# Performance work log

Hardware: AMD Instinct MI355X
Metric: run time of the kernel (lower is better)

Reference implementation:

```python
import jax, jax.numpy as jnp
import numpy as np

B, N, DIM = 2, 2048, 512
HEADS, DIM_HEAD = 8, 64
INNER = HEADS * DIM_HEAD
SCALE = DIM_HEAD ** -0.5
ALPHA = 32.0 ** 2  # stable_softmax alpha


def setup_inputs() -> dict:
    key = jax.random.key(0)
    k1, k2, k3, k4 = jax.random.split(key, 4)
    x = jax.random.normal(k1, (B, N, DIM), dtype=jnp.float32)
    mask = jnp.ones((B, N), dtype=bool)
    # nn.Linear(dim, inner*3, bias=False) -> stored transposed for x @ W
    w_qkv = jax.random.normal(k2, (DIM, INNER * 3), dtype=jnp.float32) * (DIM ** -0.5)
    w_out = jax.random.normal(k3, (INNER, DIM), dtype=jnp.float32) * (INNER ** -0.5)
    b_out = jax.random.normal(k4, (DIM,), dtype=jnp.float32) * 0.01
    return {"x": x, "mask": mask, "w_qkv": w_qkv, "w_out": w_out, "b_out": b_out}


def stable_softmax(t, alpha=ALPHA):
    t = t / alpha
    t = t - jnp.max(t, axis=-1, keepdims=True)
    return jax.nn.softmax(t * alpha, axis=-1)


def reference(x, mask, w_qkv, w_out, b_out):
    b, n, _ = x.shape
    qkv = x @ w_qkv  # [b, n, 3*inner]
    q, k, v = jnp.split(qkv, 3, axis=-1)
    # 'b n (h d) -> b h n d'
    split_heads = lambda t: t.reshape(b, n, HEADS, DIM_HEAD).transpose(0, 2, 1, 3)
    q, k, v = split_heads(q), split_heads(k), split_heads(v)
    q = q * SCALE
    dots = jnp.einsum('bhid,bhjd->bhij', q, k)  # [b, h, n, n]
    mask_value = -jnp.finfo(dots.dtype).max
    # key padding mask: 'b j -> b 1 1 j'
    dots = jnp.where(mask[:, None, None, :], dots, mask_value)
    # causal mask: triu with offset j - i + 1 == 1 here
    causal = jnp.triu(jnp.ones((n, n), dtype=bool), k=1)
    dots = jnp.where(causal, mask_value, dots)
    attn = stable_softmax(dots)
    out = jnp.einsum('bhij,bhjd->bhid', attn, v)
    out = out.transpose(0, 2, 1, 3).reshape(b, n, INNER)  # 'b h n d -> b n (h d)'
    return out @ w_out + b_out
```

## Files before the change

kernel.cpp:

```cpp
#include <hip/hip_runtime.h>
#include <hip/hip_bf16.h>
#include <stdint.h>

#define B_ 2
#define N_ 2048
#define DIM_ 512
#define HEADS_ 8
#define DHEAD_ 64
#define INNER_ 512

typedef float f32x4 __attribute__((ext_vector_type(4)));
typedef float f32x16 __attribute__((ext_vector_type(16)));
typedef __bf16 bf16x8 __attribute__((ext_vector_type(8)));
typedef unsigned short us8 __attribute__((ext_vector_type(8)));
typedef unsigned int u32x4 __attribute__((ext_vector_type(4)));

static __device__ __forceinline__ unsigned short f2bf(float f) {
    union { float f; unsigned int u; } v; v.f = f;
    unsigned int r = v.u + 0x7fffu + ((v.u >> 16) & 1u);
    return (unsigned short)(r >> 16);
}

static __device__ __forceinline__ float exp2_fast(float x) {
    return __builtin_amdgcn_exp2f(x);
}

static __device__ __forceinline__ unsigned cvtpk(float lo, float hi) {
    unsigned r;
    asm("v_cvt_pk_bf16_f32 %0, %1, %2" : "=v"(r) : "v"(lo), "v"(hi));
    return r;
}

static __device__ __forceinline__ f32x4 mfma16(bf16x8 a, bf16x8 b, f32x4 c) {
    return __builtin_amdgcn_mfma_f32_16x16x32_bf16(a, b, c, 0, 0, 0);
}
static __device__ __forceinline__ f32x16 mfma32(bf16x8 a, bf16x8 b, f32x16 c) {
    return __builtin_amdgcn_mfma_f32_32x32x16_bf16(a, b, c, 0, 0, 0);
}

static __device__ __forceinline__ size_t qk_off(int bh, int n, int d) {
    int T = n >> 5, r = n & 31, c = d >> 4, s = d & 15;
    return ((((size_t)bh * 64 + T) * 4 + c) << 9) + (size_t)(((s >> 3) * 32 + r) * 8 + (s & 7));
}
static __device__ __forceinline__ size_t vt_off(int bh, int d, int n) {
    int tt = n >> 5, kv = n & 31;
    int mi = (kv >> 4) & 1, g = (kv >> 2) & 1;
    int jj = (kv & 3) + 4 * ((kv >> 3) & 1);
    int dblk = d >> 5;
    int lane = (d & 31) + 32 * g;
    return ((((size_t)bh * 64 + tt) * 2 + dblk) * 2 + mi) * 512 + (size_t)(lane * 8 + jj);
}

__global__ __launch_bounds__(256) void k_transpose_w(const float* __restrict__ wqkv,
                                                     const float* __restrict__ wout,
                                                     unsigned short* __restrict__ oqkv,
                                                     unsigned short* __restrict__ oout,
                                                     float qscale) {
    __shared__ float tile[32][33];
    const int tx = threadIdx.x & 31, ty = threadIdx.x >> 5;
    const bool isQ = blockIdx.y < 48;
    const float* in = isQ ? wqkv : wout;
    unsigned short* out = isQ ? oqkv : oout;
    const int N = isQ ? 1536 : 512;
    const int scale_cols = isQ ? 512 : 0;
    const int K = 512;
    const int k0 = blockIdx.x * 32, n0 = (isQ ? blockIdx.y : blockIdx.y - 48) * 32;
#pragma unroll
    for (int j = 0; j < 4; j++)
        tile[ty + 8 * j][tx] = in[(size_t)(k0 + ty + 8 * j) * N + n0 + tx];
    __syncthreads();
#pragma unroll
    for (int j = 0; j < 4; j++) {
        int n = n0 + ty + 8 * j;
        float v = tile[tx][ty + 8 * j];
        if (n < scale_cols) v *= qscale;
        out[(size_t)n * K + k0 + tx] = f2bf(v);
    }
}

template <int MODE>
__global__ __launch_bounds__(256) void k_gemm(const void* __restrict__ Av,
                                              const unsigned short* __restrict__ Bt,
                                              int K, int Ncols,
                                              float* __restrict__ Cf,
                                              const float* __restrict__ bias,
                                              unsigned short* __restrict__ Qb,
                                              unsigned short* __restrict__ Kb,
                                              unsigned short* __restrict__ Vt) {
    __shared__ unsigned short As[128 * 72];
    __shared__ unsigned short Bs[128 * 72];
    const int t = threadIdx.x;
    const int lane = t & 63;
    const int w = t >> 6;
    const int wy = w >> 1, wx = w & 1;
    const int lo = lane & 15, hi = lane >> 4;

    const int ncolb = Ncols >> 7;
    const int bid = blockIdx.x;
    const int wg = (bid & 7) * ((int)gridDim.x >> 3) + (bid >> 3);
    const int row0 = (wg / ncolb) * 128, col0 = (wg % ncolb) * 128;

    f32x4 acc[4][4];
#pragma unroll
    for (int m = 0; m < 4; m++)
#pragma unroll
        for (int n = 0; n < 4; n++) acc[m][n] = 0.f;

    for (int k0 = 0; k0 < K; k0 += 64) {
#pragma unroll
        for (int i = 0; i < 4; i++) {
            int chunk = t + i * 256;
            int r = chunk >> 3;
            int c = (chunk & 7) << 3;
            if (MODE == 0) {
                const float* Af = (const float*)Av;
                float4 v0 = *(const float4*)&Af[(size_t)(row0 + r) * K + k0 + c];
                float4 v1 = *(const float4*)&Af[(size_t)(row0 + r) * K + k0 + c + 4];
                us8 o;
                o[0] = f2bf(v0.x); o[1] = f2bf(v0.y); o[2] = f2bf(v0.z); o[3] = f2bf(v0.w);
                o[4] = f2bf(v1.x); o[5] = f2bf(v1.y); o[6] = f2bf(v1.z); o[7] = f2bf(v1.w);
                *(us8*)&As[r * 72 + c] = o;
            } else {
                const unsigned short* Ab = (const unsigned short*)Av;
                *(us8*)&As[r * 72 + c] = *(const us8*)&Ab[(size_t)(row0 + r) * K + k0 + c];
            }
            *(us8*)&Bs[r * 72 + c] = *(const us8*)&Bt[(size_t)(col0 + r) * K + k0 + c];
        }
        __syncthreads();
#pragma unroll
        for (int ks = 0; ks < 2; ks++) {
            bf16x8 af[4], bfr[4];
#pragma unroll
            for (int m = 0; m < 4; m++)
                af[m] = *(const bf16x8*)&As[(wy * 64 + m * 16 + lo) * 72 + ks * 32 + hi * 8];
#pragma unroll
            for (int n = 0; n < 4; n++)
                bfr[n] = *(const bf16x8*)&Bs[(wx * 64 + n * 16 + lo) * 72 + ks * 32 + hi * 8];
#pragma unroll
            for (int m = 0; m < 4; m++)
#pragma unroll
                for (int n = 0; n < 4; n++)
                    acc[m][n] = mfma16(af[m], bfr[n], acc[m][n]);
        }
        __syncthreads();
    }

#pragma unroll
    for (int m = 0; m < 4; m++) {
#pragma unroll
        for (int n = 0; n < 4; n++) {
#pragma unroll
            for (int r = 0; r < 4; r++) {
                int row = row0 + wy * 64 + m * 16 + hi * 4 + r;
                int col = col0 + wx * 64 + n * 16 + lo;
                float v = acc[m][n][r];
                if (MODE == 0) {
                    unsigned short bv = f2bf(v);
                    int b = row >> 11, nn = row & 2047;
                    int sec = col >> 9, cc = col & 511;
                    int h = cc >> 6, d = cc & 63;
                    int bh = b * HEADS_ + h;
                    if (sec == 0)      Qb[qk_off(bh, nn, d)] = bv;
                    else if (sec == 1) Kb[qk_off(bh, nn, d)] = bv;
                    else               Vt[vt_off(bh, d, nn)] = bv;
                } else {
                    Cf[(size_t)row * Ncols + col] = v + bias[col];
                }
            }
        }
    }
}


static __device__ __forceinline__ void pack_P(const f32x16& sT, bf16x8& P0, bf16x8& P1) {
    u32x4 pw0, pw1;
    pw0[0] = cvtpk(sT[0], sT[1]);   pw0[1] = cvtpk(sT[2], sT[3]);
    pw0[2] = cvtpk(sT[4], sT[5]);   pw0[3] = cvtpk(sT[6], sT[7]);
    pw1[0] = cvtpk(sT[8], sT[9]);   pw1[1] = cvtpk(sT[10], sT[11]);
    pw1[2] = cvtpk(sT[12], sT[13]); pw1[3] = cvtpk(sT[14], sT[15]);
    P0 = __builtin_bit_cast(bf16x8, pw0);
    P1 = __builtin_bit_cast(bf16x8, pw1);
}

static __device__ __forceinline__ void do_tile(
    const unsigned short* kbase, const unsigned short* vbase, int tt,
    bool diag, int qg, int half,
    const bf16x8 (&qf)[4],
    float& m_, float& l_, f32x16& o0, f32x16& o1) {
    const unsigned short* kp = kbase + (size_t)tt * 2048;
    bf16x8 kf0 = *(const bf16x8*)(kp);
    bf16x8 kf1 = *(const bf16x8*)(kp + 512);
    bf16x8 kf2 = *(const bf16x8*)(kp + 1024);
    bf16x8 kf3 = *(const bf16x8*)(kp + 1536);
    const unsigned short* vp = vbase + (size_t)tt * 2048;
    bf16x8 vf00 = *(const bf16x8*)(vp);
    bf16x8 vf01 = *(const bf16x8*)(vp + 512);
    bf16x8 vf10 = *(const bf16x8*)(vp + 1024);
    bf16x8 vf11 = *(const bf16x8*)(vp + 1536);

    f32x16 sT = 0.f;
    sT = mfma32(kf0, qf[0], sT);
    sT = mfma32(kf1, qf[1], sT);
    sT = mfma32(kf2, qf[2], sT);
    sT = mfma32(kf3, qf[3], sT);

    if (diag) {
        const int kv0 = tt * 32;
#pragma unroll
        for (int r = 0; r < 16; r++) {
            int kv = kv0 + (r & 3) + 8 * (r >> 2) + 4 * half;
            if (kv > qg) sT[r] = -1e30f;
        }
    }

    float a0 = fmaxf(sT[0], sT[1]),  a1 = fmaxf(sT[2], sT[3]);
    float a2 = fmaxf(sT[4], sT[5]),  a3 = fmaxf(sT[6], sT[7]);
    float a4 = fmaxf(sT[8], sT[9]),  a5 = fmaxf(sT[10], sT[11]);
    float a6 = fmaxf(sT[12], sT[13]), a7 = fmaxf(sT[14], sT[15]);
    float mx = fmaxf(fmaxf(fmaxf(a0, a1), fmaxf(a2, a3)),
                     fmaxf(fmaxf(a4, a5), fmaxf(a6, a7)));

    bool need = __any(mx > m_ + 11.f);
    if (need) {
        mx = fmaxf(mx, __shfl_xor(mx, 32, 64));
        float mn = fmaxf(m_, mx);
        float al = exp2_fast(m_ - mn);
        m_ = mn;
        l_ *= al;
#pragma unroll
        for (int r = 0; r < 16; r++) { o0[r] *= al; o1[r] *= al; }
    }

#pragma unroll
    for (int r = 0; r < 16; r++) sT[r] = exp2_fast(sT[r] - m_);
    float b0 = sT[0] + sT[1],   b1 = sT[2] + sT[3];
    float b2 = sT[4] + sT[5],   b3 = sT[6] + sT[7];
    float b4 = sT[8] + sT[9],   b5 = sT[10] + sT[11];
    float b6 = sT[12] + sT[13], b7 = sT[14] + sT[15];
    l_ += ((b0 + b1) + (b2 + b3)) + ((b4 + b5) + (b6 + b7));

    bf16x8 P0, P1;
    pack_P(sT, P0, P1);
    o0 = mfma32(vf00, P0, o0);
    o0 = mfma32(vf01, P1, o0);
    o1 = mfma32(vf10, P0, o1);
    o1 = mfma32(vf11, P1, o1);
}

static __device__ __forceinline__ void publish_merge(
    float (*Osh)[32 * 65], float (*Msh)[32], float (*Lsh)[64],
    int t, int w, int q31, int half, int bh, int q0,
    float m_, float l_, const f32x16& o0, const f32x16& o1,
    unsigned short* __restrict__ attb) {
    float* ow = Osh[w];
#pragma unroll
    for (int r = 0; r < 16; r++) {
        int d = (r & 3) + 8 * (r >> 2) + 4 * half;
        ow[q31 * 65 + d] = o0[r];
        ow[q31 * 65 + 32 + d] = o1[r];
    }
    Lsh[w][half * 32 + q31] = l_;
    if (half == 0) Msh[w][q31] = m_;
    __syncthreads();
    if (t < 256) {
        const int mq = t >> 3, d0 = (t & 7) * 8;
        float mg = -1e30f;
#pragma unroll
        for (int w2 = 0; w2 < 8; w2++) mg = fmaxf(mg, Msh[w2][mq]);
        float Lg = 0.f;
        float acc[8];
#pragma unroll
        for (int i = 0; i < 8; i++) acc[i] = 0.f;
#pragma unroll
        for (int w2 = 0; w2 < 8; w2++) {
            float f = exp2_fast(Msh[w2][mq] - mg);
            Lg += (Lsh[w2][mq] + Lsh[w2][32 + mq]) * f;
#pragma unroll
            for (int i = 0; i < 8; i++) acc[i] += Osh[w2][mq * 65 + d0 + i] * f;
        }
        float inv = 1.f / Lg;
        us8 ov;
#pragma unroll
        for (int i = 0; i < 8; i++) ov[i] = f2bf(acc[i] * inv);
        const int b = bh >> 3, h = bh & 7;
        *(us8*)&attb[((size_t)b * N_ + q0 + mq) * INNER_ + h * DHEAD_ + d0] = ov;
    }
    __syncthreads();
}

__global__ __launch_bounds__(512, 4) void k_attn(const unsigned short* __restrict__ Qb,
                                                 const unsigned short* __restrict__ Kb,
                                                 const unsigned short* __restrict__ Vt,
                                                 unsigned short* __restrict__ attb) {
    __shared__ float Osh[8][32 * 65];
    __shared__ float Msh[8][32];
    __shared__ float Lsh[8][64];
    const int t = threadIdx.x, lane = t & 63, w = t >> 6;
    const int q31 = lane & 31, half = lane >> 5;

    int wg = (blockIdx.x & 7) * 64 + (blockIdx.x >> 3);
    const int bh = wg >> 5;
    const int pa = wg & 31;
    const int pb = 63 - pa;

    const unsigned short* kbase = Kb + (size_t)bh * 131072 + lane * 8;
    const unsigned short* vbase = Vt + (size_t)bh * 131072 + lane * 8;
    const unsigned short* qbh   = Qb + (size_t)bh * 131072 + lane * 8;

#pragma unroll
    for (int s = 0; s < 2; s++) {
        const int p = s ? pb : pa;
        const int q0 = p * 32, qg = q0 + q31;
        const unsigned short* qp = qbh + (size_t)p * 2048;
        bf16x8 qf[4];
        qf[0] = *(const bf16x8*)(qp);
        qf[1] = *(const bf16x8*)(qp + 512);
        qf[2] = *(const bf16x8*)(qp + 1024);
        qf[3] = *(const bf16x8*)(qp + 1536);
        float m_ = -1e30f, l_ = 0.f;
        f32x16 o0 = 0.f, o1 = 0.f;
        for (int tt = w; tt <= p; tt += 8)
            do_tile(kbase, vbase, tt, tt == p, qg, half, qf, m_, l_, o0, o1);
        publish_merge(Osh, Msh, Lsh, t, w, q31, half, bh, q0, m_, l_, o0, o1, attb);
    }
}

extern "C" void kernel_launch(void* const* d_in, const int* in_sizes, int n_in,
                              void* d_out, int out_size, void* d_ws, size_t ws_size,
                              hipStream_t stream) {
    const float* x     = (const float*)d_in[0];
    const float* w_qkv = (const float*)d_in[2];
    const float* w_out = (const float*)d_in[3];
    const float* b_out = (const float*)d_in[4];
    float* out = (float*)d_out;

    char* ws = (char*)d_ws;
    size_t off = 0;
    auto alloc = [&](size_t bytes) {
        void* p = ws + off;
        off += (bytes + 255) & ~(size_t)255;
        return p;
    };
    unsigned short* wqkvt = (unsigned short*)alloc((size_t)1536 * 512 * 2);
    unsigned short* woutt = (unsigned short*)alloc((size_t)512 * 512 * 2);
    unsigned short* Qb    = (unsigned short*)alloc((size_t)16 * 2048 * 64 * 2);
    unsigned short* Kb    = (unsigned short*)alloc((size_t)16 * 2048 * 64 * 2);
    unsigned short* Vt    = (unsigned short*)alloc((size_t)16 * 2048 * 64 * 2);
    unsigned short* attb  = (unsigned short*)alloc((size_t)4096 * 512 * 2);

    const float QSCALE = 0.125f * 1.44269504088896340736f;
    k_transpose_w<<<dim3(16, 64), 256, 0, stream>>>(w_qkv, w_out, wqkvt, woutt, QSCALE);
    k_gemm<0><<<384, 256, 0, stream>>>(x, wqkvt, 512, 1536, nullptr, nullptr, Qb, Kb, Vt);
    k_attn<<<512, 512, 0, stream>>>(Qb, Kb, Vt, attb);
    k_gemm<1><<<128, 256, 0, stream>>>(attb, woutt, 512, 512, out, b_out, nullptr, nullptr, nullptr);
}
```

Measured before the change: 61.21 us.

## Split attention blocks to one query tile each and halve merge LDS buffer

Each attention workgroup now handles a single 32-query tile instead of a balanced pair (pa, 63-pa), doubling the grid to 1024 blocks, with heaviest tiles scheduled first. The cross-wave merge buffer is halved by writing o0 and o1 in two passes through a 32x33 shared array, which cuts LDS use so more workgroups can be resident per CU. The trade-off is losing the paired causal load balancing in exchange for finer-grained scheduling, plus an extra barrier round and repeated exp2 in the merge.

```diff
diff --git a/kernel.cpp b/kernel.cpp
--- a/kernel.cpp
+++ b/kernel.cpp
@@ -13,6 +13,7 @@
 typedef float f32x16 __attribute__((ext_vector_type(16)));
 typedef __bf16 bf16x8 __attribute__((ext_vector_type(8)));
 typedef unsigned short us8 __attribute__((ext_vector_type(8)));
+typedef unsigned short us4 __attribute__((ext_vector_type(4)));
 typedef unsigned int u32x4 __attribute__((ext_vector_type(4)));
 
 static __device__ __forceinline__ unsigned short f2bf(float f) {
@@ -247,81 +248,86 @@
     o1 = mfma32(vf11, P1, o1);
 }
 
-static __device__ __forceinline__ void publish_merge(
-    float (*Osh)[32 * 65], float (*Msh)[32], float (*Lsh)[64],
-    int t, int w, int q31, int half, int bh, int q0,
-    float m_, float l_, const f32x16& o0, const f32x16& o1,
-    unsigned short* __restrict__ attb) {
-    float* ow = Osh[w];
-#pragma unroll
-    for (int r = 0; r < 16; r++) {
-        int d = (r & 3) + 8 * (r >> 2) + 4 * half;
-        ow[q31 * 65 + d] = o0[r];
-        ow[q31 * 65 + 32 + d] = o1[r];
-    }
-    Lsh[w][half * 32 + q31] = l_;
-    if (half == 0) Msh[w][q31] = m_;
-    __syncthreads();
-    if (t < 256) {
-        const int mq = t >> 3, d0 = (t & 7) * 8;
-        float mg = -1e30f;
-#pragma unroll
-        for (int w2 = 0; w2 < 8; w2++) mg = fmaxf(mg, Msh[w2][mq]);
-        float Lg = 0.f;
-        float acc[8];
-#pragma unroll
-        for (int i = 0; i < 8; i++) acc[i] = 0.f;
-#pragma unroll
-        for (int w2 = 0; w2 < 8; w2++) {
-            float f = exp2_fast(Msh[w2][mq] - mg);
-            Lg += (Lsh[w2][mq] + Lsh[w2][32 + mq]) * f;
-#pragma unroll
-            for (int i = 0; i < 8; i++) acc[i] += Osh[w2][mq * 65 + d0 + i] * f;
-        }
-        float inv = 1.f / Lg;
-        us8 ov;
-#pragma unroll
-        for (int i = 0; i < 8; i++) ov[i] = f2bf(acc[i] * inv);
-        const int b = bh >> 3, h = bh & 7;
-        *(us8*)&attb[((size_t)b * N_ + q0 + mq) * INNER_ + h * DHEAD_ + d0] = ov;
-    }
-    __syncthreads();
-}
-
 __global__ __launch_bounds__(512, 4) void k_attn(const unsigned short* __restrict__ Qb,
                                                  const unsigned short* __restrict__ Kb,
                                                  const unsigned short* __restrict__ Vt,
                                                  unsigned short* __restrict__ attb) {
-    __shared__ float Osh[8][32 * 65];
+    __shared__ float Osh[8][32 * 33];
     __shared__ float Msh[8][32];
     __shared__ float Lsh[8][64];
     const int t = threadIdx.x, lane = t & 63, w = t >> 6;
     const int q31 = lane & 31, half = lane >> 5;
 
-    int wg = (blockIdx.x & 7) * 64 + (blockIdx.x >> 3);
-    const int bh = wg >> 5;
-    const int pa = wg & 31;
-    const int pb = 63 - pa;
+    int wg = (blockIdx.x & 7) * 128 + (blockIdx.x >> 3);
+    const int bh = wg >> 6;
+    const int p = 63 - (wg & 63);
+    const int q0 = p * 32, qg = q0 + q31;
+    const int b = bh >> 3, h = bh & 7;
 
     const unsigned short* kbase = Kb + (size_t)bh * 131072 + lane * 8;
     const unsigned short* vbase = Vt + (size_t)bh * 131072 + lane * 8;
-    const unsigned short* qbh   = Qb + (size_t)bh * 131072 + lane * 8;
-
-#pragma unroll
-    for (int s = 0; s < 2; s++) {
-        const int p = s ? pb : pa;
-        const int q0 = p * 32, qg = q0 + q31;
-        const unsigned short* qp = qbh + (size_t)p * 2048;
-        bf16x8 qf[4];
-        qf[0] = *(const bf16x8*)(qp);
-        qf[1] = *(const bf16x8*)(qp + 512);
-        qf[2] = *(const bf16x8*)(qp + 1024);
-        qf[3] = *(const bf16x8*)(qp + 1536);
-        float m_ = -1e30f, l_ = 0.f;
-        f32x16 o0 = 0.f, o1 = 0.f;
-        for (int tt = w; tt <= p; tt += 8)
-            do_tile(kbase, vbase, tt, tt == p, qg, half, qf, m_, l_, o0, o1);
-        publish_merge(Osh, Msh, Lsh, t, w, q31, half, bh, q0, m_, l_, o0, o1, attb);
+    const unsigned short* qp = Qb + (size_t)bh * 131072 + (size_t)p * 2048 + lane * 8;
+
+    bf16x8 qf[4];
+    qf[0] = *(const bf16x8*)(qp);
+    qf[1] = *(const bf16x8*)(qp + 512);
+    qf[2] = *(const bf16x8*)(qp + 1024);
+    qf[3] = *(const bf16x8*)(qp + 1536);
+    float m_ = -1e30f, l_ = 0.f;
+    f32x16 o0 = 0.f, o1 = 0.f;
+    for (int tt = w; tt <= p; tt += 8)
+        do_tile(kbase, vbase, tt, tt == p, qg, half, qf, m_, l_, o0, o1);
+
+    float* ow = Osh[w];
+#pragma unroll
+    for (int r = 0; r < 16; r++) {
+        int d = (r & 3) + 8 * (r >> 2) + 4 * half;
+        ow[q31 * 33 + d] = o0[r];
+    }
+    Lsh[w][half * 32 + q31] = l_;
+    if (half == 0) Msh[w][q31] = m_;
+    __syncthreads();
+
+    float mg = -1e30f, inv = 0.f;
+    const int mq = t >> 3 & 31, d0 = (t & 7) * 4;
+    if (t < 256) {
+#pragma unroll
+        for (int w2 = 0; w2 < 8; w2++) mg = fmaxf(mg, Msh[w2][mq]);
+        float Lg = 0.f;
+        float acc[4] = {0.f, 0.f, 0.f, 0.f};
+#pragma unroll
+        for (int w2 = 0; w2 < 8; w2++) {
+            float f = exp2_fast(Msh[w2][mq] - mg);
+            Lg += (Lsh[w2][mq] + Lsh[w2][32 + mq]) * f;
+#pragma unroll
+            for (int i = 0; i < 4; i++) acc[i] += Osh[w2][mq * 33 + d0 + i] * f;
+        }
+        inv = 1.f / Lg;
+        us4 ov;
+#pragma unroll
+        for (int i = 0; i < 4; i++) ov[i] = f2bf(acc[i] * inv);
+        *(us4*)&attb[((size_t)b * N_ + q0 + mq) * INNER_ + h * DHEAD_ + d0] = ov;
+    }
+    __syncthreads();
+
+#pragma unroll
+    for (int r = 0; r < 16; r++) {
+        int d = (r & 3) + 8 * (r >> 2) + 4 * half;
+        ow[q31 * 33 + d] = o1[r];
+    }
+    __syncthreads();
+    if (t < 256) {
+        float acc[4] = {0.f, 0.f, 0.f, 0.f};
+#pragma unroll
+        for (int w2 = 0; w2 < 8; w2++) {
+            float f = exp2_fast(Msh[w2][mq] - mg);
+#pragma unroll
+            for (int i = 0; i < 4; i++) acc[i] += Osh[w2][mq * 33 + d0 + i] * f;
+        }
+        us4 ov;
+#pragma unroll
+        for (int i = 0; i < 4; i++) ov[i] = f2bf(acc[i] * inv);
+        *(us4*)&attb[((size_t)b * N_ + q0 + mq) * INNER_ + h * DHEAD_ + 32 + d0] = ov;
     }
 }
 
@@ -351,6 +357,6 @@
     const float QSCALE = 0.125f * 1.44269504088896340736f;
     k_transpose_w<<<dim3(16, 64), 256, 0, stream>>>(w_qkv, w_out, wqkvt, woutt, QSCALE);
     k_gemm<0><<<384, 256, 0, stream>>>(x, wqkvt, 512, 1536, nullptr, nullptr, Qb, Kb, Vt);
-    k_attn<<<512, 512, 0, stream>>>(Qb, Kb, Vt, attb);
+    k_attn<<<1024, 512, 0, stream>>>(Qb, Kb, Vt, attb);
     k_gemm<1><<<128, 256, 0, stream>>>(attb, woutt, 512, 512, out, b_out, nullptr, nullptr, nullptr);
 }
```

After: 64.72 us. 5.7% more time.
